# Kernel optimization log

Hardware: AMD Instinct MI355X
Metric: run time of the kernel (lower is better)

The kernel has to match this reference:

```python
import jax, jax.numpy as jnp
import numpy as np

N = 100000   # nodes
E = 1600000  # edges
F = 64       # input_features == output_features
BN_EPS = 1e-5


def _bn(x, gamma, beta):
    # torch BatchNorm1d (training mode): biased batch statistics
    mu = jnp.mean(x, axis=0)
    var = jnp.var(x, axis=0)
    return (x - mu) * jax.lax.rsqrt(var + BN_EPS) * gamma + beta


def setup_inputs() -> dict:
    key = jax.random.key(0)
    ks = jax.random.split(key, 16)
    s = 0.05
    inp = {
        'node_feats': jax.random.normal(ks[0], (N, F), jnp.float32),
        'edge_feats': jax.random.normal(ks[1], (E, F), jnp.float32),
        'src': jax.random.randint(ks[2], (E,), 0, N, jnp.int32),
        'dst': jax.random.randint(ks[3], (E,), 0, N, jnp.int32),
        # linear params: W [F_in, F_out], b [F_out]
        'W_src_gate': jax.random.normal(ks[4], (F, F), jnp.float32) * s,
        'b_src_gate': jnp.zeros((F,), jnp.float32),
        'W_dst_gate': jax.random.normal(ks[5], (F, F), jnp.float32) * s,
        'b_dst_gate': jnp.zeros((F,), jnp.float32),
        'W_edge_gate': jax.random.normal(ks[6], (F, F), jnp.float32) * s,
        'b_edge_gate': jnp.zeros((F,), jnp.float32),
        'W_src_update': jax.random.normal(ks[7], (F, F), jnp.float32) * s,
        'b_src_update': jnp.zeros((F,), jnp.float32),
        'W_dst_update': jax.random.normal(ks[8], (F, F), jnp.float32) * s,
        'b_dst_update': jnp.zeros((F,), jnp.float32),
        'bn_nodes_gamma': jnp.ones((F,), jnp.float32),
        'bn_nodes_beta': jnp.zeros((F,), jnp.float32),
        'bn_edges_gamma': jnp.ones((F,), jnp.float32),
        'bn_edges_beta': jnp.zeros((F,), jnp.float32),
    }
    return inp


def reference(node_feats, edge_feats, src, dst,
              W_src_gate, b_src_gate, W_dst_gate, b_dst_gate,
              W_edge_gate, b_edge_gate, W_src_update, b_src_update,
              W_dst_update, b_dst_update,
              bn_nodes_gamma, bn_nodes_beta, bn_edges_gamma, bn_edges_beta):
    # EdgeGatedGraphConv (arXiv:1711.07553), residual=True
    e_src = node_feats @ W_src_gate + b_src_gate          # [N,F]
    e_dst = node_feats @ W_dst_gate + b_dst_gate          # [N,F]
    # u_add_v gather + edge transform -> gate logits m [E,F]
    m = e_src[src] + e_dst[dst] + (edge_feats @ W_edge_gate + b_edge_gate)
    sigma = jax.nn.sigmoid(m)                             # [E,F]
    Bh = node_feats @ W_dst_update + b_dst_update         # [N,F]
    # u_mul_e message + scatter-sum to destination nodes
    sum_sigma_h = jax.ops.segment_sum(Bh[src] * sigma, dst, num_segments=node_feats.shape[0])
    sum_sigma = jax.ops.segment_sum(sigma, dst, num_segments=node_feats.shape[0])
    h = sum_sigma_h / (sum_sigma + 1e-6)                  # normalized aggregation
    x = node_feats @ W_src_update + b_src_update + h
    x = jax.nn.silu(_bn(x, bn_nodes_gamma, bn_nodes_beta))
    y = jax.nn.silu(_bn(m, bn_edges_gamma, bn_edges_beta))
    x = node_feats + x   # residual
    y = edge_feats + y   # residual
    return (x, y)
```

## Files before the change

kernel.cpp:

```cpp
#include <hip/hip_runtime.h>
#include <hip/hip_bf16.h>

typedef __attribute__((ext_vector_type(8))) __bf16 bf16x8;
typedef __attribute__((ext_vector_type(4))) float f32x4;

#define MFMA(a,b,c) __builtin_amdgcn_mfma_f32_16x16x32_bf16((a),(b),(c),0,0,0)

__device__ __forceinline__ bf16x8 cvt8(float4 a, float4 b){
  bf16x8 r;
  r[0]=(__bf16)a.x; r[1]=(__bf16)a.y; r[2]=(__bf16)a.z; r[3]=(__bf16)a.w;
  r[4]=(__bf16)b.x; r[5]=(__bf16)b.y; r[6]=(__bf16)b.z; r[7]=(__bf16)b.w;
  return r;
}

__global__ void zero_k(int4* __restrict__ p, int n4){
  int i = blockIdx.x*256 + threadIdx.x, st = gridDim.x*256;
  for (; i<n4; i+=st) p[i] = make_int4(0,0,0,0);
}

__global__ void wcvt(const float* __restrict__ W_sg, const float* __restrict__ W_dg,
                     const float* __restrict__ W_eg, const float* __restrict__ W_su,
                     const float* __restrict__ W_du,
                     bf16x8* __restrict__ Wp, bf16x8* __restrict__ Wq){
  int tid = blockIdx.x*256 + threadIdx.x;
  if (tid >= 2560 + 1536) return;
  int lane = tid & 63, g = lane>>4, c = lane&15;
  if (tid < 2560){
    int frag = (tid>>6)&7, m = tid>>9;
    const float* Ws[5] = {W_sg, W_dg, W_eg, W_su, W_du};
    const float* W = Ws[m];
    int kt = frag>>2, nt = frag&3;
    bf16x8 v;
    #pragma unroll
    for (int j=0;j<8;j++) v[j] = (__bf16)W[(kt*32+g*8+j)*64 + nt*16 + c];
    Wp[tid] = v;
  } else {
    int t2 = tid - 2560;
    int frag = (t2>>6)&7, m = t2>>9;
    const float* Ws[3] = {W_eg, W_sg, W_dg};
    const float* W = Ws[m];
    int mt = frag>>1, kh = frag&1;
    bf16x8 v;
    #pragma unroll
    for (int j=0;j<8;j++) v[j] = (__bf16)W[(kh*32+g*8+j)*64 + mt*16 + c];
    Wq[t2] = v;
  }
}

__global__ __launch_bounds__(256) void node_xform(
    const float* __restrict__ nf, const bf16x8* __restrict__ Wp,
    const float* __restrict__ b_su, const float* __restrict__ b_du,
    float* __restrict__ A_src, float* __restrict__ Bh, int ntiles)
{
  int lane = threadIdx.x & 63;
  int gw = blockIdx.x*4 + (threadIdx.x>>6);
  if (gw >= ntiles) return;
  int g = lane>>4, c = lane&15;
  long base = (long)gw*16;
  const float* rp = nf + (base + c)*64 + g*8;
  float4 a0 = *(const float4*)rp,      a1 = *(const float4*)(rp+4);
  float4 a2 = *(const float4*)(rp+32), a3 = *(const float4*)(rp+36);
  bf16x8 A0 = cvt8(a0,a1), A1 = cvt8(a2,a3);
  const float* biases[2] = {b_su,b_du};
  float* outs[2] = {A_src,Bh};
  const int mats[2] = {3,4};
  #pragma unroll
  for (int i=0;i<2;i++){
    #pragma unroll
    for (int nt=0;nt<4;nt++){
      f32x4 acc = {0.f,0.f,0.f,0.f};
      acc = MFMA(A0, Wp[(mats[i]*8+nt)*64+lane],   acc);
      acc = MFMA(A1, Wp[(mats[i]*8+4+nt)*64+lane], acc);
      int col = c + nt*16;
      float bb = biases[i][col];
      #pragma unroll
      for (int e=0;e<4;e++) outs[i][(base+4*g+e)*64 + col] = acc[e] + bb;
    }
  }
}

__global__ void hist_k(const int* __restrict__ dst, int* __restrict__ cnt, int E){
  int i = blockIdx.x*256 + threadIdx.x, st = gridDim.x*256;
  for (; i<E; i+=st) atomicAdd(&cnt[dst[i]], 1);
}

__global__ __launch_bounds__(1024) void scan_k(const int* __restrict__ cnt,
                                               int* __restrict__ row, int Nn){
  __shared__ int part[1024];
  int t = threadIdx.x;
  int C = (Nn + 1023) >> 10;
  int lo = t*C;
  int hi = lo + C; if (hi > Nn) hi = Nn;
  int s = 0;
  for (int i=lo; i<hi; i++) s += cnt[i];
  part[t] = s;
  __syncthreads();
  for (int off=1; off<1024; off<<=1){
    int v = part[t];
    int u = (t>=off) ? part[t-off] : 0;
    __syncthreads();
    part[t] = v + u;
    __syncthreads();
  }
  int excl = (t==0) ? 0 : part[t-1];
  for (int i=lo; i<hi; i++){ row[i] = excl; excl += cnt[i]; }
  if (t==1023) row[Nn] = excl;
}

__global__ void fill_k(const int* __restrict__ src, const int* __restrict__ dst,
                       const int* __restrict__ rowp, int* __restrict__ cnt2,
                       int2* __restrict__ pairs, int E){
  int i = blockIdx.x*256 + threadIdx.x, st = gridDim.x*256;
  for (; i<E; i+=st){
    int d = dst[i];
    int pos = rowp[d] + atomicAdd(&cnt2[d], 1);
    pairs[pos] = make_int2(i, src[i]);
  }
}

__global__ __launch_bounds__(256) void phaseA(
    const float* __restrict__ ef, const float* __restrict__ nf,
    const int* __restrict__ src, const int* __restrict__ dst,
    const float* __restrict__ b_sg, const float* __restrict__ b_dg,
    const float* __restrict__ b_eg,
    const bf16x8* __restrict__ Wq,
    __bf16* __restrict__ m16, int ntiles)
{
  __shared__ bf16x8 wl[24*64];
  {
    int t = threadIdx.x;
    #pragma unroll
    for (int i=0;i<6;i++) wl[i*256+t] = Wq[i*256+t];
  }
  __syncthreads();
  int lane = threadIdx.x & 63, g = lane>>4, c = lane&15;
  int gw = blockIdx.x*4 + (threadIdx.x>>6);
  int nw = gridDim.x*4;
  float bias2[4][4];
  #pragma unroll
  for (int mt=0;mt<4;mt++)
    #pragma unroll
    for (int e=0;e<4;e++){
      int f = mt*16 + 4*g + e;
      bias2[mt][e] = b_sg[f] + b_dg[f] + b_eg[f];
    }
  int sc = 0, dc = 0;
  if (gw < ntiles){ sc = src[(long)gw*16 + c]; dc = dst[(long)gw*16 + c]; }
  for (int tt=gw; tt<ntiles; tt+=nw){
    long base = (long)tt*16;
    int tn = tt + nw;
    int sn = sc, dn = dc;
    if (tn < ntiles){ sn = src[(long)tn*16 + c]; dn = dst[(long)tn*16 + c]; }
    const float* rpe = ef + (base+c)*64 + g*8;
    const float* rps = nf + (long)sc*64 + g*8;
    const float* rpd = nf + (long)dc*64 + g*8;
    float4 e0=*(const float4*)rpe,      e1=*(const float4*)(rpe+4);
    float4 e2=*(const float4*)(rpe+32), e3=*(const float4*)(rpe+36);
    float4 s0=*(const float4*)rps,      s1=*(const float4*)(rps+4);
    float4 s2=*(const float4*)(rps+32), s3=*(const float4*)(rps+36);
    float4 d0=*(const float4*)rpd,      d1=*(const float4*)(rpd+4);
    float4 d2=*(const float4*)(rpd+32), d3=*(const float4*)(rpd+36);
    bf16x8 BE0=cvt8(e0,e1), BE1=cvt8(e2,e3);
    bf16x8 BS0=cvt8(s0,s1), BS1=cvt8(s2,s3);
    bf16x8 BD0=cvt8(d0,d1), BD1=cvt8(d2,d3);
    #pragma unroll
    for (int mt=0;mt<4;mt++){
      f32x4 am = {0.f,0.f,0.f,0.f};
      am = MFMA(wl[((0*4+mt)*2+0)*64+lane], BE0, am);
      am = MFMA(wl[((0*4+mt)*2+1)*64+lane], BE1, am);
      am = MFMA(wl[((1*4+mt)*2+0)*64+lane], BS0, am);
      am = MFMA(wl[((1*4+mt)*2+1)*64+lane], BS1, am);
      am = MFMA(wl[((2*4+mt)*2+0)*64+lane], BD0, am);
      am = MFMA(wl[((2*4+mt)*2+1)*64+lane], BD1, am);
      union { __bf16 h[4]; uint2 u; } pk;
      #pragma unroll
      for (int e=0;e<4;e++) pk.h[e] = (__bf16)(am[e] + bias2[mt][e]);
      *(uint2*)(m16 + (base+c)*64 + mt*16 + 4*g) = pk.u;
    }
    sc = sn; dc = dn;
  }
}

__global__ __launch_bounds__(256) void phaseB(
    const __bf16* __restrict__ m16, const int2* __restrict__ pairs,
    const float* __restrict__ Bh, const int* __restrict__ rowp,
    float* __restrict__ A_src,
    float* __restrict__ est, float* __restrict__ nst, int Nn)
{
  __shared__ float sst[256];
  sst[threadIdx.x] = 0.f;
  __syncthreads();
  int lane = threadIdx.x & 63, w = threadIdx.x>>6;
  int chunk = (Nn + gridDim.x - 1)/gridDim.x;
  int n0 = blockIdx.x*chunk;
  int n1 = n0 + chunk; if (n1 > Nn) n1 = Nn;
  float e1=0.f, e2=0.f, p1=0.f, p2=0.f;
  for (int n=n0+w; n<n1; n+=4){
    int r0 = rowp[n], r1 = rowp[n+1];
    float ssum=0.f, bsum=0.f;
    int r = r0;
    for (; r+8 <= r1; r+=8){
      int2 q[8];
      #pragma unroll
      for (int j=0;j<8;j++) q[j] = pairs[r+j];
      float mv[8], bh[8];
      #pragma unroll
      for (int j=0;j<8;j++) mv[j] = (float)m16[(long)q[j].x*64 + lane];
      #pragma unroll
      for (int j=0;j<8;j++) bh[j] = Bh[(long)q[j].y*64 + lane];
      #pragma unroll
      for (int j=0;j<8;j++){
        float sg = 1.f/(1.f+__expf(-mv[j]));
        ssum += sg; bsum += bh[j]*sg;
        e1 += mv[j]; e2 += mv[j]*mv[j];
      }
    }
    for (; r < r1; ++r){
      int2 q0 = pairs[r];
      float mv0 = (float)m16[(long)q0.x*64 + lane];
      float bh0 = Bh[(long)q0.y*64 + lane];
      float sg0 = 1.f/(1.f+__expf(-mv0));
      ssum += sg0; bsum += bh0*sg0;
      e1 += mv0;   e2 += mv0*mv0;
    }
    long xi = (long)n*64 + lane;
    float xp = A_src[xi] + bsum/(ssum+1e-6f);
    A_src[xi] = xp;
    p1 += xp; p2 += xp*xp;
  }
  atomicAdd(&sst[lane],     e1);
  atomicAdd(&sst[64+lane],  e2);
  atomicAdd(&sst[128+lane], p1);
  atomicAdd(&sst[192+lane], p2);
  __syncthreads();
  int t = threadIdx.x;
  if (t < 128) atomicAdd(&est[t], sst[t]);
  else         atomicAdd(&nst[t-128], sst[t]);
}

__global__ __launch_bounds__(256) void node_final(
    const float* __restrict__ nf, const float* __restrict__ xpre,
    const float* __restrict__ nst, const float* __restrict__ gam,
    const float* __restrict__ bet, float* __restrict__ xo, int Nn)
{
  long tid = blockIdx.x*blockDim.x + threadIdx.x;
  long stride = (long)gridDim.x*blockDim.x;
  int col = (int)(tid & 63);
  float invN = 1.f/(float)Nn;
  float mu = nst[col]*invN;
  float var = nst[64+col]*invN - mu*mu;
  float rs = rsqrtf(var + 1e-5f);
  float aa = gam[col]*rs;
  float bb = bet[col] - mu*aa;
  long total = (long)Nn*64;
  for (long i=tid; i<total; i+=stride){
    float z = xpre[i]*aa + bb;
    xo[i] = nf[i] + z/(1.f+__expf(-z));
  }
}

__global__ __launch_bounds__(256) void edge_final(
    const __bf16* __restrict__ m16, const float* __restrict__ ef,
    const float* __restrict__ est, const float* __restrict__ gam,
    const float* __restrict__ bet, float* __restrict__ y, float invE, long E)
{
  int oct = threadIdx.x & 7;
  float aa[8], bb[8];
  #pragma unroll
  for (int j=0;j<8;j++){
    int col = oct*8 + j;
    float mu = est[col]*invE;
    float var = est[64+col]*invE - mu*mu;
    float rs = rsqrtf(var + 1e-5f);
    float ga = gam[col]*rs;
    aa[j] = ga; bb[j] = bet[col] - mu*ga;
  }
  long tid = (long)blockIdx.x*256 + threadIdx.x;
  long pstep = ((long)gridDim.x*256) >> 3;
  for (long p = tid>>3; p < E; p += pstep){
    bf16x8 mv = *(const bf16x8*)&m16[p*64 + oct*8];
    const float* rp = ef + p*64 + oct*8;
    float4 f0 = *(const float4*)rp, f1 = *(const float4*)(rp+4);
    float o[8];
    #pragma unroll
    for (int j=0;j<8;j++){
      float z = aa[j]*(float)mv[j] + bb[j];
      float ev = (j<4) ? ((const float*)&f0)[j] : ((const float*)&f1)[j-4];
      o[j] = ev + z/(1.f+__expf(-z));
    }
    float* yp = y + p*64 + oct*8;
    *(float4*)yp     = make_float4(o[0],o[1],o[2],o[3]);
    *(float4*)(yp+4) = make_float4(o[4],o[5],o[6],o[7]);
  }
}

extern "C" void kernel_launch(void* const* d_in, const int* in_sizes, int n_in,
                              void* d_out, int out_size, void* d_ws, size_t ws_size,
                              hipStream_t stream){
  const float* nf  = (const float*)d_in[0];
  const float* ef  = (const float*)d_in[1];
  const int*   src = (const int*)d_in[2];
  const int*   dst = (const int*)d_in[3];
  const float* W_sg=(const float*)d_in[4];  const float* b_sg=(const float*)d_in[5];
  const float* W_dg=(const float*)d_in[6];  const float* b_dg=(const float*)d_in[7];
  const float* W_eg=(const float*)d_in[8];  const float* b_eg=(const float*)d_in[9];
  const float* W_su=(const float*)d_in[10]; const float* b_su=(const float*)d_in[11];
  const float* W_du=(const float*)d_in[12]; const float* b_du=(const float*)d_in[13];
  const float* gn=(const float*)d_in[14];   const float* btn=(const float*)d_in[15];
  const float* ge=(const float*)d_in[16];   const float* bte=(const float*)d_in[17];

  int Nn = in_sizes[0]/64;
  int Ee = in_sizes[2];
  size_t Nf = (size_t)Nn*64;
  size_t Es = (size_t)Ee;

  float* ws    = (float*)d_ws;
  float* A_src = ws;
  float* Bh    = ws + Nf;
  __bf16* m16  = (__bf16*)(ws + 2*Nf);
  int2*  pairs = (int2*)(ws + 2*Nf + 32*Es);
  int*   cnt   = (int*)(pairs + Es);
  int*   cnt2  = cnt + Nn;
  float* est   = (float*)(cnt2 + Nn);
  float* nst   = est + 128;
  int*   rowp  = (int*)(nst + 128);
  size_t woff  = 2*Nf + 32*Es + 2*Es + 2*(size_t)Nn + 256 + (size_t)Nn + 1;
  woff = (woff + 15) & ~(size_t)15;
  bf16x8* Wp   = (bf16x8*)(ws + woff);
  bf16x8* Wq   = Wp + 2560;

  float* xo = (float*)d_out;
  float* yo = xo + Nf;

  int nz4 = (int)((2*(size_t)Nn + 256) >> 2);
  zero_k<<<256,256,0,stream>>>((int4*)cnt, nz4);

  wcvt<<<16,256,0,stream>>>(W_sg,W_dg,W_eg,W_su,W_du,Wp,Wq);

  int ntn = Nn/16;
  node_xform<<<(ntn+3)/4,256,0,stream>>>(nf,Wp,b_su,b_du,A_src,Bh,ntn);
  hist_k<<<2048,256,0,stream>>>(dst,cnt,Ee);
  scan_k<<<1,1024,0,stream>>>(cnt,rowp,Nn);
  fill_k<<<2048,256,0,stream>>>(src,dst,rowp,cnt2,pairs,Ee);
  int nte = Ee/16;
  phaseA<<<4096,256,0,stream>>>(ef,nf,src,dst,b_sg,b_dg,b_eg,Wq,m16,nte);
  phaseB<<<4096,256,0,stream>>>(m16,pairs,Bh,rowp,A_src,est,nst,Nn);
  node_final<<<2048,256,0,stream>>>(nf,A_src,nst,gn,btn,xo,Nn);
  edge_final<<<4096,256,0,stream>>>(m16,ef,est,ge,bte,yo,
                                    1.f/(float)Ee,(long)Ee);
}
```

Baseline: 962.4 us.

## Merge independent kernels into block-partitioned combined launches

Pairs of independent kernels now share one launch, with the work split by block index: weight conversion with zeroing, node transform with the dst histogram, CSR fill with the edge gate computation, and node final with edge final. This removes launch gaps and lets independent work run at the same time on the GPU. In exchange, fill blocks now run beside phaseA blocks, which allocate shared memory they do not use, and the fixed block partitions may leave the two halves unevenly balanced.

```diff
diff --git a/kernel.cpp b/kernel.cpp
--- a/kernel.cpp
+++ b/kernel.cpp
@@ -13,75 +13,78 @@
   return r;
 }
 
-__global__ void zero_k(int4* __restrict__ p, int n4){
-  int i = blockIdx.x*256 + threadIdx.x, st = gridDim.x*256;
-  for (; i<n4; i+=st) p[i] = make_int4(0,0,0,0);
-}
-
-__global__ void wcvt(const float* __restrict__ W_sg, const float* __restrict__ W_dg,
-                     const float* __restrict__ W_eg, const float* __restrict__ W_su,
-                     const float* __restrict__ W_du,
-                     bf16x8* __restrict__ Wp, bf16x8* __restrict__ Wq){
-  int tid = blockIdx.x*256 + threadIdx.x;
-  if (tid >= 2560 + 1536) return;
-  int lane = tid & 63, g = lane>>4, c = lane&15;
-  if (tid < 2560){
-    int frag = (tid>>6)&7, m = tid>>9;
-    const float* Ws[5] = {W_sg, W_dg, W_eg, W_su, W_du};
-    const float* W = Ws[m];
-    int kt = frag>>2, nt = frag&3;
-    bf16x8 v;
-    #pragma unroll
-    for (int j=0;j<8;j++) v[j] = (__bf16)W[(kt*32+g*8+j)*64 + nt*16 + c];
-    Wp[tid] = v;
+__global__ void setup_k(const float* __restrict__ W_sg, const float* __restrict__ W_dg,
+                        const float* __restrict__ W_eg, const float* __restrict__ W_su,
+                        const float* __restrict__ W_du,
+                        bf16x8* __restrict__ Wp, bf16x8* __restrict__ Wq,
+                        int4* __restrict__ zp, int nz4){
+  if (blockIdx.x < 16){
+    int tid = blockIdx.x*256 + threadIdx.x;
+    if (tid >= 2560 + 1536) return;
+    int lane = tid & 63, g = lane>>4, c = lane&15;
+    if (tid < 2560){
+      int frag = (tid>>6)&7, m = tid>>9;
+      const float* Ws[5] = {W_sg, W_dg, W_eg, W_su, W_du};
+      const float* W = Ws[m];
+      int kt = frag>>2, nt = frag&3;
+      bf16x8 v;
+      #pragma unroll
+      for (int j=0;j<8;j++) v[j] = (__bf16)W[(kt*32+g*8+j)*64 + nt*16 + c];
+      Wp[tid] = v;
+    } else {
+      int t2 = tid - 2560;
+      int frag = (t2>>6)&7, m = t2>>9;
+      const float* Ws[3] = {W_eg, W_sg, W_dg};
+      const float* W = Ws[m];
+      int mt = frag>>1, kh = frag&1;
+      bf16x8 v;
+      #pragma unroll
+      for (int j=0;j<8;j++) v[j] = (__bf16)W[(kh*32+g*8+j)*64 + mt*16 + c];
+      Wq[t2] = v;
+    }
   } else {
-    int t2 = tid - 2560;
-    int frag = (t2>>6)&7, m = t2>>9;
-    const float* Ws[3] = {W_eg, W_sg, W_dg};
-    const float* W = Ws[m];
-    int mt = frag>>1, kh = frag&1;
-    bf16x8 v;
-    #pragma unroll
-    for (int j=0;j<8;j++) v[j] = (__bf16)W[(kh*32+g*8+j)*64 + mt*16 + c];
-    Wq[t2] = v;
-  }
-}
-
-__global__ __launch_bounds__(256) void node_xform(
+    int i = (blockIdx.x-16)*256 + threadIdx.x, st = (gridDim.x-16)*256;
+    for (; i<nz4; i+=st) zp[i] = make_int4(0,0,0,0);
+  }
+}
+
+__global__ __launch_bounds__(256) void xform_hist_k(
     const float* __restrict__ nf, const bf16x8* __restrict__ Wp,
     const float* __restrict__ b_su, const float* __restrict__ b_du,
-    float* __restrict__ A_src, float* __restrict__ Bh, int ntiles)
+    float* __restrict__ A_src, float* __restrict__ Bh, int ntiles, int nxf,
+    const int* __restrict__ dst, int* __restrict__ cnt, int E)
 {
-  int lane = threadIdx.x & 63;
-  int gw = blockIdx.x*4 + (threadIdx.x>>6);
-  if (gw >= ntiles) return;
-  int g = lane>>4, c = lane&15;
-  long base = (long)gw*16;
-  const float* rp = nf + (base + c)*64 + g*8;
-  float4 a0 = *(const float4*)rp,      a1 = *(const float4*)(rp+4);
-  float4 a2 = *(const float4*)(rp+32), a3 = *(const float4*)(rp+36);
-  bf16x8 A0 = cvt8(a0,a1), A1 = cvt8(a2,a3);
-  const float* biases[2] = {b_su,b_du};
-  float* outs[2] = {A_src,Bh};
-  const int mats[2] = {3,4};
-  #pragma unroll
-  for (int i=0;i<2;i++){
-    #pragma unroll
-    for (int nt=0;nt<4;nt++){
-      f32x4 acc = {0.f,0.f,0.f,0.f};
-      acc = MFMA(A0, Wp[(mats[i]*8+nt)*64+lane],   acc);
-      acc = MFMA(A1, Wp[(mats[i]*8+4+nt)*64+lane], acc);
-      int col = c + nt*16;
-      float bb = biases[i][col];
-      #pragma unroll
-      for (int e=0;e<4;e++) outs[i][(base+4*g+e)*64 + col] = acc[e] + bb;
-    }
-  }
-}
-
-__global__ void hist_k(const int* __restrict__ dst, int* __restrict__ cnt, int E){
-  int i = blockIdx.x*256 + threadIdx.x, st = gridDim.x*256;
-  for (; i<E; i+=st) atomicAdd(&cnt[dst[i]], 1);
+  if ((int)blockIdx.x < nxf){
+    int lane = threadIdx.x & 63;
+    int gw = blockIdx.x*4 + (threadIdx.x>>6);
+    if (gw >= ntiles) return;
+    int g = lane>>4, c = lane&15;
+    long base = (long)gw*16;
+    const float* rp = nf + (base + c)*64 + g*8;
+    float4 a0 = *(const float4*)rp,      a1 = *(const float4*)(rp+4);
+    float4 a2 = *(const float4*)(rp+32), a3 = *(const float4*)(rp+36);
+    bf16x8 A0 = cvt8(a0,a1), A1 = cvt8(a2,a3);
+    const float* biases[2] = {b_su,b_du};
+    float* outs[2] = {A_src,Bh};
+    const int mats[2] = {3,4};
+    #pragma unroll
+    for (int i=0;i<2;i++){
+      #pragma unroll
+      for (int nt=0;nt<4;nt++){
+        f32x4 acc = {0.f,0.f,0.f,0.f};
+        acc = MFMA(A0, Wp[(mats[i]*8+nt)*64+lane],   acc);
+        acc = MFMA(A1, Wp[(mats[i]*8+4+nt)*64+lane], acc);
+        int col = c + nt*16;
+        float bb = biases[i][col];
+        #pragma unroll
+        for (int e=0;e<4;e++) outs[i][(base+4*g+e)*64 + col] = acc[e] + bb;
+      }
+    }
+  } else {
+    int nb = gridDim.x - nxf;
+    int i = (blockIdx.x-nxf)*256 + threadIdx.x, st = nb*256;
+    for (; i<E; i+=st) atomicAdd(&cnt[dst[i]], 1);
+  }
 }
 
 __global__ __launch_bounds__(1024) void scan_k(const int* __restrict__ cnt,
@@ -107,26 +110,27 @@
   if (t==1023) row[Nn] = excl;
 }
 
-__global__ void fill_k(const int* __restrict__ src, const int* __restrict__ dst,
-                       const int* __restrict__ rowp, int* __restrict__ cnt2,
-                       int2* __restrict__ pairs, int E){
-  int i = blockIdx.x*256 + threadIdx.x, st = gridDim.x*256;
-  for (; i<E; i+=st){
-    int d = dst[i];
-    int pos = rowp[d] + atomicAdd(&cnt2[d], 1);
-    pairs[pos] = make_int2(i, src[i]);
-  }
-}
-
-__global__ __launch_bounds__(256) void phaseA(
+#define NFILL 1024
+__global__ __launch_bounds__(256) void fillA_k(
+    const int* __restrict__ src, const int* __restrict__ dst,
+    const int* __restrict__ rowp, int* __restrict__ cnt2,
+    int2* __restrict__ pairs, int E,
     const float* __restrict__ ef, const float* __restrict__ nf,
-    const int* __restrict__ src, const int* __restrict__ dst,
     const float* __restrict__ b_sg, const float* __restrict__ b_dg,
     const float* __restrict__ b_eg,
     const bf16x8* __restrict__ Wq,
     __bf16* __restrict__ m16, int ntiles)
 {
   __shared__ bf16x8 wl[24*64];
+  if (blockIdx.x < NFILL){
+    int i = blockIdx.x*256 + threadIdx.x, st = NFILL*256;
+    for (; i<E; i+=st){
+      int d = dst[i];
+      int pos = rowp[d] + atomicAdd(&cnt2[d], 1);
+      pairs[pos] = make_int2(i, src[i]);
+    }
+    return;
+  }
   {
     int t = threadIdx.x;
     #pragma unroll
@@ -134,8 +138,8 @@
   }
   __syncthreads();
   int lane = threadIdx.x & 63, g = lane>>4, c = lane&15;
-  int gw = blockIdx.x*4 + (threadIdx.x>>6);
-  int nw = gridDim.x*4;
+  int gw = (blockIdx.x-NFILL)*4 + (threadIdx.x>>6);
+  int nw = (gridDim.x-NFILL)*4;
   float bias2[4][4];
   #pragma unroll
   for (int mt=0;mt<4;mt++)
@@ -238,59 +242,59 @@
   else         atomicAdd(&nst[t-128], sst[t]);
 }
 
-__global__ __launch_bounds__(256) void node_final(
+#define NNF 1024
+__global__ __launch_bounds__(256) void finals_k(
     const float* __restrict__ nf, const float* __restrict__ xpre,
-    const float* __restrict__ nst, const float* __restrict__ gam,
-    const float* __restrict__ bet, float* __restrict__ xo, int Nn)
+    const float* __restrict__ nst, const float* __restrict__ gn,
+    const float* __restrict__ btn, float* __restrict__ xo, int Nn,
+    const __bf16* __restrict__ m16, const float* __restrict__ ef,
+    const float* __restrict__ est, const float* __restrict__ ge,
+    const float* __restrict__ bte, float* __restrict__ y, float invE, long E)
 {
-  long tid = blockIdx.x*blockDim.x + threadIdx.x;
-  long stride = (long)gridDim.x*blockDim.x;
-  int col = (int)(tid & 63);
-  float invN = 1.f/(float)Nn;
-  float mu = nst[col]*invN;
-  float var = nst[64+col]*invN - mu*mu;
-  float rs = rsqrtf(var + 1e-5f);
-  float aa = gam[col]*rs;
-  float bb = bet[col] - mu*aa;
-  long total = (long)Nn*64;
-  for (long i=tid; i<total; i+=stride){
-    float z = xpre[i]*aa + bb;
-    xo[i] = nf[i] + z/(1.f+__expf(-z));
-  }
-}
-
-__global__ __launch_bounds__(256) void edge_final(
-    const __bf16* __restrict__ m16, const float* __restrict__ ef,
-    const float* __restrict__ est, const float* __restrict__ gam,
-    const float* __restrict__ bet, float* __restrict__ y, float invE, long E)
-{
-  int oct = threadIdx.x & 7;
-  float aa[8], bb[8];
-  #pragma unroll
-  for (int j=0;j<8;j++){
-    int col = oct*8 + j;
-    float mu = est[col]*invE;
-    float var = est[64+col]*invE - mu*mu;
+  if (blockIdx.x < NNF){
+    long tid = (long)blockIdx.x*256 + threadIdx.x;
+    long stride = (long)NNF*256;
+    int col = (int)(tid & 63);
+    float invN = 1.f/(float)Nn;
+    float mu = nst[col]*invN;
+    float var = nst[64+col]*invN - mu*mu;
     float rs = rsqrtf(var + 1e-5f);
-    float ga = gam[col]*rs;
-    aa[j] = ga; bb[j] = bet[col] - mu*ga;
-  }
-  long tid = (long)blockIdx.x*256 + threadIdx.x;
-  long pstep = ((long)gridDim.x*256) >> 3;
-  for (long p = tid>>3; p < E; p += pstep){
-    bf16x8 mv = *(const bf16x8*)&m16[p*64 + oct*8];
-    const float* rp = ef + p*64 + oct*8;
-    float4 f0 = *(const float4*)rp, f1 = *(const float4*)(rp+4);
-    float o[8];
+    float aa = gn[col]*rs;
+    float bb = btn[col] - mu*aa;
+    long total = (long)Nn*64;
+    for (long i=tid; i<total; i+=stride){
+      float z = xpre[i]*aa + bb;
+      xo[i] = nf[i] + z/(1.f+__expf(-z));
+    }
+  } else {
+    int oct = threadIdx.x & 7;
+    float aa[8], bb[8];
     #pragma unroll
     for (int j=0;j<8;j++){
-      float z = aa[j]*(float)mv[j] + bb[j];
-      float ev = (j<4) ? ((const float*)&f0)[j] : ((const float*)&f1)[j-4];
-      o[j] = ev + z/(1.f+__expf(-z));
-    }
-    float* yp = y + p*64 + oct*8;
-    *(float4*)yp     = make_float4(o[0],o[1],o[2],o[3]);
-    *(float4*)(yp+4) = make_float4(o[4],o[5],o[6],o[7]);
+      int col = oct*8 + j;
+      float mu = est[col]*invE;
+      float var = est[64+col]*invE - mu*mu;
+      float rs = rsqrtf(var + 1e-5f);
+      float ga = ge[col]*rs;
+      aa[j] = ga; bb[j] = bte[col] - mu*ga;
+    }
+    long tid = (long)(blockIdx.x-NNF)*256 + threadIdx.x;
+    long pstep = ((long)(gridDim.x-NNF)*256) >> 3;
+    for (long p = tid>>3; p < E; p += pstep){
+      bf16x8 mv = *(const bf16x8*)&m16[p*64 + oct*8];
+      const float* rp = ef + p*64 + oct*8;
+      float4 f0 = *(const float4*)rp, f1 = *(const float4*)(rp+4);
+      float o[8];
+      #pragma unroll
+      for (int j=0;j<8;j++){
+        float z = aa[j]*(float)mv[j] + bb[j];
+        float ev = (j<4) ? ((const float*)&f0)[j] : ((const float*)&f1)[j-4];
+        o[j] = ev + z/(1.f+__expf(-z));
+      }
+      float* yp = y + p*64 + oct*8;
+      *(float4*)yp     = make_float4(o[0],o[1],o[2],o[3]);
+      *(float4*)(yp+4) = make_float4(o[4],o[5],o[6],o[7]);
+    }
   }
 }
 
@@ -333,19 +337,18 @@
   float* yo = xo + Nf;
 
   int nz4 = (int)((2*(size_t)Nn + 256) >> 2);
-  zero_k<<<256,256,0,stream>>>((int4*)cnt, nz4);
-
-  wcvt<<<16,256,0,stream>>>(W_sg,W_dg,W_eg,W_su,W_du,Wp,Wq);
+  setup_k<<<272,256,0,stream>>>(W_sg,W_dg,W_eg,W_su,W_du,Wp,Wq,(int4*)cnt,nz4);
 
   int ntn = Nn/16;
-  node_xform<<<(ntn+3)/4,256,0,stream>>>(nf,Wp,b_su,b_du,A_src,Bh,ntn);
-  hist_k<<<2048,256,0,stream>>>(dst,cnt,Ee);
+  int nxf = (ntn+3)/4;
+  xform_hist_k<<<nxf+2048,256,0,stream>>>(nf,Wp,b_su,b_du,A_src,Bh,ntn,nxf,
+                                          dst,cnt,Ee);
   scan_k<<<1,1024,0,stream>>>(cnt,rowp,Nn);
-  fill_k<<<2048,256,0,stream>>>(src,dst,rowp,cnt2,pairs,Ee);
   int nte = Ee/16;
-  phaseA<<<4096,256,0,stream>>>(ef,nf,src,dst,b_sg,b_dg,b_eg,Wq,m16,nte);
+  fillA_k<<<NFILL+4096,256,0,stream>>>(src,dst,rowp,cnt2,pairs,Ee,
+                                       ef,nf,b_sg,b_dg,b_eg,Wq,m16,nte);
   phaseB<<<4096,256,0,stream>>>(m16,pairs,Bh,rowp,A_src,est,nst,Nn);
-  node_final<<<2048,256,0,stream>>>(nf,A_src,nst,gn,btn,xo,Nn);
-  edge_final<<<4096,256,0,stream>>>(m16,ef,est,ge,bte,yo,
-                                    1.f/(float)Ee,(long)Ee);
-}
+  finals_k<<<NNF+4096,256,0,stream>>>(nf,A_src,nst,gn,btn,xo,Nn,
+                                      m16,ef,est,ge,bte,yo,
+                                      1.f/(float)Ee,(long)Ee);
+}
```

Measured after the change: 932.2 us. 1.03x faster.
